# Kernel tuning notes

Measured on AMD Instinct MI355X. Metric: run time of the kernel, lower is better.

The kernel has to match this reference:

```python
import jax, jax.numpy as jnp
import numpy as np

K = 255
L = 1.0 / K
W = L / 2.5
MU = (L * (jnp.arange(K, dtype=jnp.float32) + 0.5))  # [K]


def soft_hist(x):
    # x: [B, H, W] -> [B, K] soft histogram (mean of sigmoid-window memberships)
    B = x.shape[0]
    N = x.shape[1] * x.shape[2]
    xf = x.reshape(B, 1, -1)                      # [B, 1, N]
    d = xf - MU[None, :, None]                    # [B, K, N]
    pj = jax.nn.sigmoid((d + L / 2) / W) - jax.nn.sigmoid((d - L / 2) / W)
    return pj.sum(axis=2) / N                     # [B, K]


def emd(x, y):
    # matmul with lower-triangular ones == cumulative sum along bins
    cdf_x = jnp.cumsum(x, axis=1)
    cdf_y = jnp.cumsum(y, axis=1)
    return jnp.sum(jnp.square(cdf_x - cdf_y), axis=1)  # [B]


def setup_inputs() -> dict:
    key = jax.random.key(0)
    k1, k2 = jax.random.split(key)
    img = jax.random.uniform(k1, (8, 3, 256, 256), dtype=jnp.float32)
    img_t = jax.random.uniform(k2, (8, 3, 256, 256), dtype=jnp.float32)
    return {"img": img, "img_t": img_t}


def reference(img, img_t):
    r, g, b = img[:, 0], img[:, 1], img[:, 2]
    r_t, g_t, b_t = img_t[:, 0], img_t[:, 1], img_t[:, 2]
    r_hist = soft_hist(r)
    g_hist = soft_hist(g)
    b_hist = soft_hist(b)
    r_t_hist = soft_hist(r_t)  # computed but unused, faithful to original (bug: earth(r_hist, r_hist))
    g_t_hist = soft_hist(g_t)
    b_t_hist = soft_hist(b_t)
    loss = emd(r_hist, r_hist) + emd(g_hist, g_t_hist) + emd(b_hist, b_t_hist)
    return loss  # [B]
```

## Files before the change

### kernel.cpp

```cpp
#include <hip/hip_runtime.h>


#define QF 16
#define FBINS 4096
#define FBV 4080
#define PADL 64
#define CNTSZ (PADL + FBINS + 64)

__device__ __forceinline__ float fsigmoid(float z) {
    return __builtin_amdgcn_rcpf(1.0f + __expf(-z));
}

template<int SUB>
__global__ __launch_bounds__(256) void fine_hist_kernel(
    const float* __restrict__ img, const float* __restrict__ img_t,
    unsigned* __restrict__ part)
{
    const int blk = blockIdx.x;
    const int h   = blk / SUB;
    const int s   = blk - h * SUB;
    const int b   = h >> 2;
    const int ch  = 1 + ((h >> 1) & 1);
    const float* src = (h & 1) ? img_t : img;
    const int pix = 65536 / SUB;
    const float4* base = (const float4*)(src + (size_t)(b * 3 + ch) * 65536u
                                             + (size_t)s * (size_t)pix);

    __shared__ unsigned hist[FBINS];
    uint4* h4 = (uint4*)hist;
    #pragma unroll
    for (int r = 0; r < 4; ++r)
        h4[threadIdx.x + 256 * r] = make_uint4(0u, 0u, 0u, 0u);
    __syncthreads();

    const int nv = pix >> 2;
    for (int i = threadIdx.x; i < nv; i += 256) {
        const float4 v = base[i];
        int j0 = (int)(v.x * 4080.0f);
        int j1 = (int)(v.y * 4080.0f);
        int j2 = (int)(v.z * 4080.0f);
        int j3 = (int)(v.w * 4080.0f);
        j0 = j0 < 0 ? 0 : (j0 > FBV - 1 ? FBV - 1 : j0);
        j1 = j1 < 0 ? 0 : (j1 > FBV - 1 ? FBV - 1 : j1);
        j2 = j2 < 0 ? 0 : (j2 > FBV - 1 ? FBV - 1 : j2);
        j3 = j3 < 0 ? 0 : (j3 > FBV - 1 ? FBV - 1 : j3);
        atomicAdd(&hist[j0], 1u);
        atomicAdd(&hist[j1], 1u);
        atomicAdd(&hist[j2], 1u);
        atomicAdd(&hist[j3], 1u);
    }
    __syncthreads();

    uint4* o = (uint4*)(part + (size_t)blk * (size_t)FBINS);
    #pragma unroll
    for (int r = 0; r < 4; ++r)
        o[threadIdx.x + 256 * r] = h4[threadIdx.x + 256 * r];
}

template<int SUB>
__global__ __launch_bounds__(256) void merge_kernel(
    const unsigned* __restrict__ part, unsigned* __restrict__ merged)
{
    const int h = blockIdx.x >> 3;
    const int c = blockIdx.x & 7;
    const int t = threadIdx.x;
    const unsigned* p0 = part + (size_t)h * SUB * FBINS + c * 512 + 2 * t;
    unsigned ax = 0u, ay = 0u;
    #pragma unroll
    for (int s = 0; s < SUB; ++s) {
        const uint2 u = *(const uint2*)(p0 + (size_t)s * FBINS);
        ax += u.x; ay += u.y;
    }
    *(uint2*)(merged + (size_t)h * FBINS + c * 512 + 2 * t) = make_uint2(ax, ay);
}

__global__ __launch_bounds__(1024) void cdf_emd_kernel(
    const unsigned* __restrict__ merged, float* __restrict__ out)
{
    const int b   = blockIdx.x;
    const int tid = threadIdx.x;
    const int sg  = tid >> 8;
    const int k   = tid & 255;

    __shared__ float cnt[4][CNTSZ];
    __shared__ float coarse[4][256];
    __shared__ float sgt[128];
    __shared__ float s0red[16];
    __shared__ float cdfs[4][256];
    __shared__ float lred[16];

    if (tid < 128)
        sgt[tid] = fsigmoid((2.5f / 16.0f) * ((float)tid + 0.5f) - 10.0f);

    const uint4* src = (const uint4*)(merged + (size_t)(b * 4 + sg) * FBINS);
    float* cn = cnt[sg];
    #pragma unroll
    for (int r = 0; r < 4; ++r) {
        const uint4 u = src[k + 256 * r];
        *(float4*)(cn + PADL + 4 * (k + 256 * r)) =
            make_float4((float)u.x, (float)u.y, (float)u.z, (float)u.w);
    }
    if (k < PADL) cn[k] = 0.0f;
    if (k < CNTSZ - PADL - FBINS) cn[PADL + FBINS + k] = 0.0f;
    __syncthreads();

    float cc = 0.0f;
    #pragma unroll
    for (int q = 0; q < QF; ++q) {
        const int qq = (q + k) & (QF - 1);
        cc += cn[PADL + QF * k + qq];
    }
    coarse[sg][k] = cc;

    float s0p = 0.0f;
    if (k < 64) s0p = cn[PADL + k] * fsigmoid((2.5f / 16.0f) * ((float)k + 0.5f));
    #pragma unroll
    for (int off = 32; off; off >>= 1) s0p += __shfl_down(s0p, off);
    if ((tid & 63) == 0) s0red[tid >> 6] = s0p;
    __syncthreads();
    const float S0w = s0red[4 * sg] + s0red[4 * sg + 1]
                    + s0red[4 * sg + 2] + s0red[4 * sg + 3];

    for (int off = 1; off < 256; off <<= 1) {
        const float v = (k + off < 256) ? coarse[sg][k + off] : 0.0f;
        __syncthreads();
        coarse[sg][k] += v;
        __syncthreads();
    }
    const float S0 = S0w + coarse[sg][4];

    float t = 0.0f;
    const int jb = PADL + QF * k - 48;
    for (int i = 0; i < 128; ++i) {
        const int m = (i + k) & 127;
        t += cn[jb + m] * sgt[m];
    }
    const float ones = (k + 5 < 256) ? coarse[sg][k + 5] : 0.0f;

    cdfs[sg][k] = (k <= 254) ? (S0 - t - ones) * (1.0f / 65536.0f) : 0.0f;
    __syncthreads();

    if (tid < 256) {
        const float dg = cdfs[0][tid] - cdfs[1][tid];
        const float db = cdfs[2][tid] - cdfs[3][tid];
        float v = dg * dg + db * db;
        #pragma unroll
        for (int off = 32; off; off >>= 1) v += __shfl_down(v, off);
        if ((tid & 63) == 0) lred[tid >> 6] = v;
    }
    __syncthreads();
    if (tid == 0) out[b] = lred[0] + lred[1] + lred[2] + lred[3];
}

template<int SUB>
static void launch_all(const float* img, const float* img_t, float* out,
                       void* d_ws, hipStream_t stream)
{
    unsigned* part   = (unsigned*)d_ws;
    unsigned* merged = part + (size_t)32 * SUB * FBINS;
    hipLaunchKernelGGL(fine_hist_kernel<SUB>, dim3(32 * SUB), dim3(256), 0, stream,
                       img, img_t, part);
    hipLaunchKernelGGL(merge_kernel<SUB>, dim3(256), dim3(256), 0, stream,
                       part, merged);
    hipLaunchKernelGGL(cdf_emd_kernel, dim3(8), dim3(1024), 0, stream,
                       merged, out);
}

extern "C" void kernel_launch(void* const* d_in, const int* in_sizes, int n_in,
                              void* d_out, int out_size, void* d_ws, size_t ws_size,
                              hipStream_t stream)
{
    const float* img   = (const float*)d_in[0];
    const float* img_t = (const float*)d_in[1];
    float* out = (float*)d_out;

    const size_t need16 = ((size_t)32 * 16 + 32) * FBINS * 4u;
    const size_t need4  = ((size_t)32 * 4  + 32) * FBINS * 4u;

    if (ws_size >= need16)      launch_all<16>(img, img_t, out, d_ws, stream);
    else if (ws_size >= need4)  launch_all<4>(img, img_t, out, d_ws, stream);
    else                        launch_all<1>(img, img_t, out, d_ws, stream);
}
```

Baseline: 74.57 us.

## Merge histogram partials with packed 16-bit global atomics instead of merge kernel

```diff
diff --git a/kernel.cpp b/kernel.cpp
--- a/kernel.cpp
+++ b/kernel.cpp
@@ -11,31 +11,33 @@
     return __builtin_amdgcn_rcpf(1.0f + __expf(-z));
 }
 
-template<int SUB>
-__global__ __launch_bounds__(256) void fine_hist_kernel(
+__global__ __launch_bounds__(256) void zero_kernel(uint4* __restrict__ p) {
+    p[blockIdx.x * 256 + threadIdx.x] = make_uint4(0u, 0u, 0u, 0u);
+}
+
+__global__ __launch_bounds__(512) void fine_hist_kernel(
     const float* __restrict__ img, const float* __restrict__ img_t,
-    unsigned* __restrict__ part)
+    unsigned long long* __restrict__ merged)
 {
     const int blk = blockIdx.x;
-    const int h   = blk / SUB;
-    const int s   = blk - h * SUB;
+    const int h   = blk >> 3;
+    const int s   = blk & 7;
     const int b   = h >> 2;
     const int ch  = 1 + ((h >> 1) & 1);
     const float* src = (h & 1) ? img_t : img;
-    const int pix = 65536 / SUB;
     const float4* base = (const float4*)(src + (size_t)(b * 3 + ch) * 65536u
-                                             + (size_t)s * (size_t)pix);
+                                             + (size_t)s * 8192u);
 
     __shared__ unsigned hist[FBINS];
     uint4* h4 = (uint4*)hist;
     #pragma unroll
-    for (int r = 0; r < 4; ++r)
-        h4[threadIdx.x + 256 * r] = make_uint4(0u, 0u, 0u, 0u);
+    for (int r = 0; r < 2; ++r)
+        h4[threadIdx.x + 512 * r] = make_uint4(0u, 0u, 0u, 0u);
     __syncthreads();
 
-    const int nv = pix >> 2;
-    for (int i = threadIdx.x; i < nv; i += 256) {
-        const float4 v = base[i];
+    #pragma unroll
+    for (int r = 0; r < 4; ++r) {
+        const float4 v = base[threadIdx.x + 512 * r];
         int j0 = (int)(v.x * 4080.0f);
         int j1 = (int)(v.y * 4080.0f);
         int j2 = (int)(v.z * 4080.0f);
@@ -51,31 +53,20 @@
     }
     __syncthreads();
 
-    uint4* o = (uint4*)(part + (size_t)blk * (size_t)FBINS);
-    #pragma unroll
-    for (int r = 0; r < 4; ++r)
-        o[threadIdx.x + 256 * r] = h4[threadIdx.x + 256 * r];
-}
-
-template<int SUB>
-__global__ __launch_bounds__(256) void merge_kernel(
-    const unsigned* __restrict__ part, unsigned* __restrict__ merged)
-{
-    const int h = blockIdx.x >> 3;
-    const int c = blockIdx.x & 7;
-    const int t = threadIdx.x;
-    const unsigned* p0 = part + (size_t)h * SUB * FBINS + c * 512 + 2 * t;
-    unsigned ax = 0u, ay = 0u;
-    #pragma unroll
-    for (int s = 0; s < SUB; ++s) {
-        const uint2 u = *(const uint2*)(p0 + (size_t)s * FBINS);
-        ax += u.x; ay += u.y;
+    unsigned long long* dst = merged + (size_t)h * 1024u;
+    for (int j = threadIdx.x; j < 1024; j += 512) {
+        const uint4 u = h4[j];
+        const unsigned long long v =
+              (unsigned long long)u.x
+            | ((unsigned long long)u.y << 16)
+            | ((unsigned long long)u.z << 32)
+            | ((unsigned long long)u.w << 48);
+        if (v) atomicAdd(&dst[j], v);
     }
-    *(uint2*)(merged + (size_t)h * FBINS + c * 512 + 2 * t) = make_uint2(ax, ay);
 }
 
 __global__ __launch_bounds__(1024) void cdf_emd_kernel(
-    const unsigned* __restrict__ merged, float* __restrict__ out)
+    const unsigned long long* __restrict__ merged, float* __restrict__ out)
 {
     const int b   = blockIdx.x;
     const int tid = threadIdx.x;
@@ -92,13 +83,14 @@
     if (tid < 128)
         sgt[tid] = fsigmoid((2.5f / 16.0f) * ((float)tid + 0.5f) - 10.0f);
 
-    const uint4* src = (const uint4*)(merged + (size_t)(b * 4 + sg) * FBINS);
+    const uint2* src = (const uint2*)(merged + (size_t)(b * 4 + sg) * 1024u);
     float* cn = cnt[sg];
     #pragma unroll
     for (int r = 0; r < 4; ++r) {
-        const uint4 u = src[k + 256 * r];
+        const uint2 u = src[k + 256 * r];
         *(float4*)(cn + PADL + 4 * (k + 256 * r)) =
-            make_float4((float)u.x, (float)u.y, (float)u.z, (float)u.w);
+            make_float4((float)(u.x & 0xffffu), (float)(u.x >> 16),
+                        (float)(u.y & 0xffffu), (float)(u.y >> 16));
     }
     if (k < PADL) cn[k] = 0.0f;
     if (k < CNTSZ - PADL - FBINS) cn[PADL + FBINS + k] = 0.0f;
@@ -152,20 +144,6 @@
     if (tid == 0) out[b] = lred[0] + lred[1] + lred[2] + lred[3];
 }
 
-template<int SUB>
-static void launch_all(const float* img, const float* img_t, float* out,
-                       void* d_ws, hipStream_t stream)
-{
-    unsigned* part   = (unsigned*)d_ws;
-    unsigned* merged = part + (size_t)32 * SUB * FBINS;
-    hipLaunchKernelGGL(fine_hist_kernel<SUB>, dim3(32 * SUB), dim3(256), 0, stream,
-                       img, img_t, part);
-    hipLaunchKernelGGL(merge_kernel<SUB>, dim3(256), dim3(256), 0, stream,
-                       part, merged);
-    hipLaunchKernelGGL(cdf_emd_kernel, dim3(8), dim3(1024), 0, stream,
-                       merged, out);
-}
-
 extern "C" void kernel_launch(void* const* d_in, const int* in_sizes, int n_in,
                               void* d_out, int out_size, void* d_ws, size_t ws_size,
                               hipStream_t stream)
@@ -174,10 +152,12 @@
     const float* img_t = (const float*)d_in[1];
     float* out = (float*)d_out;
 
-    const size_t need16 = ((size_t)32 * 16 + 32) * FBINS * 4u;
-    const size_t need4  = ((size_t)32 * 4  + 32) * FBINS * 4u;
+    unsigned long long* merged = (unsigned long long*)d_ws;
 
-    if (ws_size >= need16)      launch_all<16>(img, img_t, out, d_ws, stream);
-    else if (ws_size >= need4)  launch_all<4>(img, img_t, out, d_ws, stream);
-    else                        launch_all<1>(img, img_t, out, d_ws, stream);
+    hipLaunchKernelGGL(zero_kernel, dim3(64), dim3(256), 0, stream,
+                       (uint4*)merged);
+    hipLaunchKernelGGL(fine_hist_kernel, dim3(256), dim3(512), 0, stream,
+                       img, img_t, merged);
+    hipLaunchKernelGGL(cdf_emd_kernel, dim3(8), dim3(1024), 0, stream,
+                       merged, out);
 }
```

After: 72.43 us. -2.9%, faster.
